# Optimization experiments

Measured on AMD Instinct MI355X. Metric: run time of the kernel, lower is better.

Reference implementation:

```python
import jax, jax.numpy as jnp
import numpy as np

B, N, D_MODEL, H, BLK = 2, 2048, 1024, 16, 128
TB = N // BLK  # 16 blocks per side
NEG = -1e30


def setup_inputs() -> dict:
    key = jax.random.key(0)
    kq, kk, kv, kb = jax.random.split(key, 4)
    q = jax.random.normal(kq, (B, N, D_MODEL), jnp.float32)
    k = jax.random.normal(kk, (B, N, D_MODEL), jnp.float32)
    v = jax.random.normal(kv, (B, N, D_MODEL), jnp.float32)
    tau = jnp.float32(1.0)
    mask = jnp.ones((B, 1, N, N), jnp.int32)
    block_sparse_mask = jax.random.randint(kb, (TB, TB), 0, 2).astype(jnp.int32)
    return {"q": q, "k": k, "v": v, "tau": tau, "mask": mask,
            "block_sparse_mask": block_sparse_mask}


def reference(q, k, v, tau, mask, block_sparse_mask):
    # Equivalent closed form of the tiled online-softmax loop (dropout p=0, eval
    # mode): processed blocks accumulate exactly masked softmax(tau*QK^T/sqrt(dk))@V;
    # rows whose every block is skipped keep O=0, l=0, m=-inf.
    Bq, Nq, D = q.shape
    d_k = D // H
    qh = q.reshape(Bq, Nq, H, d_k).transpose(0, 2, 1, 3)  # (B,H,N,dk)
    kh = k.reshape(Bq, Nq, H, d_k).transpose(0, 2, 1, 3)
    vh = v.reshape(Bq, Nq, H, d_k).transpose(0, 2, 1, 3)

    S = tau * jnp.einsum('bhqd,bhkd->bhqk', qh, kh) / np.sqrt(d_k).astype(np.float32)

    # expand block-sparse pattern to token resolution (N,N)
    bs = jnp.repeat(jnp.repeat(block_sparse_mask, BLK, axis=0), BLK, axis=1)
    allowed = (mask != 0) & (bs != 0)  # (B,1,N,N), broadcasts over heads

    S_m = jnp.where(allowed, S, NEG)
    m = jnp.max(S_m, axis=-1, keepdims=True)            # (B,H,N,1)
    P = jnp.exp(S_m - m) * allowed.astype(S.dtype)      # masked exp-weights
    l = jnp.sum(P, axis=-1, keepdims=True)              # (B,H,N,1)
    Ov = jnp.einsum('bhqk,bhkd->bhqd', P, vh)
    O = Ov / jnp.where(l > 0, l, 1.0)

    has_any = jnp.any(allowed, axis=-1, keepdims=True)  # (B,1,N,1)
    m_out = jnp.where(has_any, m, -jnp.inf)
    O_out = O.transpose(0, 2, 1, 3).reshape(Bq, Nq, D)
    return O_out, l, m_out
```

## Files before the change

### kernel.cpp

```cpp
#include <hip/hip_runtime.h>
#include <hip/hip_bf16.h>

#define B_   2
#define N_   2048
#define DM_  1024
#define H_   16
#define DK_  64
#define BLK_ 128
#define TB_  16

typedef unsigned short u16;
typedef unsigned int   u32;
using bf16x8 = __attribute__((ext_vector_type(8))) __bf16;
using f32x4  = __attribute__((ext_vector_type(4))) float;

#define PPAD 136
#define OPAD 68

__device__ __forceinline__ u32 pack_bf16(float a, float b) {
  __hip_bfloat162 h = __float22bfloat162_rn(make_float2(a, b));
  u32 u; __builtin_memcpy(&u, &h, 4); return u;
}
__device__ __forceinline__ bf16x8 pack8(float4 f0, float4 f1, float sc) {
  u32 w[4];
  w[0] = pack_bf16(f0.x * sc, f0.y * sc); w[1] = pack_bf16(f0.z * sc, f0.w * sc);
  w[2] = pack_bf16(f1.x * sc, f1.y * sc); w[3] = pack_bf16(f1.z * sc, f1.w * sc);
  bf16x8 r; __builtin_memcpy(&r, w, 16); return r;
}

__global__ void prepass_kernel(const float* __restrict__ k, const float* __restrict__ v,
                               const int* __restrict__ mask, const int* __restrict__ bs,
                               u16* __restrict__ kimg, u16* __restrict__ vimg,
                               int* __restrict__ flags) {
  __shared__ u16 tile[BLK_][DK_ + 2];
  __shared__ int sAll[4], sAny[4];
  const int blk0 = blockIdx.x;
  const int t = threadIdx.x;
  if (blk0 < 512) {
    const int nb = blk0 & 15, h = (blk0 >> 4) & 15, b = blk0 >> 8;
    const size_t obase = ((size_t)((b * H_ + h) * TB_ + nb)) * 8192;
    const int rr = t >> 4, cc = (t & 15) * 4;
    {
      const float* kg = k + ((size_t)(b * N_ + nb * BLK_)) * DM_ + h * DK_;
      u16* kd = kimg + obase;
#pragma unroll
      for (int i = 0; i < 8; ++i) {
        const int r = rr + i * 16;
        const float4 f = *(const float4*)(kg + (size_t)r * DM_ + cc);
        const int so = ((((cc >> 3) ^ (r & 7)) << 3) | (cc & 4));
        *(uint2*)(kd + r * 64 + so) = make_uint2(pack_bf16(f.x, f.y), pack_bf16(f.z, f.w));
      }
    }
    {
      const float* vg = v + ((size_t)(b * N_ + nb * BLK_)) * DM_ + h * DK_;
#pragma unroll
      for (int i = 0; i < 8; ++i) {
        const int r = rr + i * 16;
        const float4 f = *(const float4*)(vg + (size_t)r * DM_ + cc);
        *(u32*)(&tile[r][cc])     = pack_bf16(f.x, f.y);
        *(u32*)(&tile[r][cc + 2]) = pack_bf16(f.z, f.w);
      }
      __syncthreads();
      const int d = t & 63, n0 = (t >> 6) * 32;
      u16* og = vimg + obase + d * 128;
#pragma unroll
      for (int j = 0; j < 32; j += 8) {
        u16 tmp[8];
#pragma unroll
        for (int x = 0; x < 8; ++x) tmp[x] = tile[n0 + j + x][d];
        uint4 w; __builtin_memcpy(&w, tmp, 16);
        const int chunk = (n0 + j) >> 3;
        *(uint4*)(og + ((chunk ^ (d & 7)) << 3)) = w;
      }
    }
  } else {
    const int blk = blk0 - 512;
    const int kb = blk % TB_, qb = (blk / TB_) % TB_, b = blk / (TB_ * TB_);
    const int* mg = mask + (size_t)b * N_ * N_ + (size_t)(qb * BLK_) * N_ + kb * BLK_;
    int all1 = 1, any1 = 0;
    for (int i = t; i < BLK_ * BLK_ / 4; i += 256) {
      const int r = i >> 5, c = (i & 31) * 4;
      const int4 mv = *(const int4*)(mg + (size_t)r * N_ + c);
      all1 &= (mv.x != 0) & (mv.y != 0) & (mv.z != 0) & (mv.w != 0);
      any1 |= (mv.x != 0) | (mv.y != 0) | (mv.z != 0) | (mv.w != 0);
    }
    const int wv = t >> 6;
    const int wAll = __all(all1), wAny = __any(any1);
    if ((t & 63) == 0) { sAll[wv] = wAll; sAny[wv] = wAny; }
    __syncthreads();
    if (t == 0) {
      const int A = sAll[0] & sAll[1] & sAll[2] & sAll[3];
      const int O = sAny[0] | sAny[1] | sAny[2] | sAny[3];
      int f = 0;
      if (bs[qb * TB_ + kb] != 0 && O) f = A ? 1 : 2;
      flags[blk] = f;
    }
  }
}

#define SOFTMAX_PHASE(stA, NT) do {                                              \
    if (mix) {                                                                   \
      const int* mg = mask + (size_t)b * N_ * N_ + (size_t)qg[NT] * N_ + cur * BLK_; \
      _Pragma("unroll")                                                          \
      for (int kt = 0; kt < 8; ++kt) {                                           \
        const int4 mv = *(const int4*)(mg + kt * 16 + quad * 4);                 \
        if (!mv.x) stA[kt][0] = -1e30f;                                          \
        if (!mv.y) stA[kt][1] = -1e30f;                                          \
        if (!mv.z) stA[kt][2] = -1e30f;                                          \
        if (!mv.w) stA[kt][3] = -1e30f;                                          \
      }                                                                          \
    }                                                                            \
    float mx = -INFINITY;                                                        \
    _Pragma("unroll")                                                            \
    for (int kt = 0; kt < 8; ++kt)                                               \
      mx = fmaxf(mx, fmaxf(fmaxf(stA[kt][0], stA[kt][1]),                        \
                           fmaxf(stA[kt][2], stA[kt][3])));                      \
    mx = fmaxf(mx, __shfl_xor(mx, 16, 64));                                      \
    mx = fmaxf(mx, __shfl_xor(mx, 32, 64));                                      \
    m_true[NT] = fmaxf(m_true[NT], mx);                                          \
    const float mold = m_run[NT];                                                \
    float mnew = mold;                                                           \
    if (!__all(mx <= mold + 8.f)) {                                              \
      mnew = fmaxf(mold, mx);                                                    \
      const float alpha = __builtin_amdgcn_exp2f(mold - mnew);                   \
      l_run[NT] *= alpha;                                                        \
      _Pragma("unroll")                                                          \
      for (int mt = 0; mt < 4; ++mt)                                             \
        _Pragma("unroll")                                                        \
        for (int r = 0; r < 4; ++r) oacc[NT][mt][r] *= alpha;                    \
      m_run[NT] = mnew;                                                          \
    }                                                                            \
    const int qloc = wave * 32 + NT * 16 + col;                                  \
    float s = 0.f;                                                               \
    if (!mix) {                                                                  \
      _Pragma("unroll")                                                          \
      for (int kt = 0; kt < 8; ++kt) {                                           \
        const float p0 = __builtin_amdgcn_exp2f(stA[kt][0] - mnew);              \
        const float p1 = __builtin_amdgcn_exp2f(stA[kt][1] - mnew);              \
        const float p2 = __builtin_amdgcn_exp2f(stA[kt][2] - mnew);              \
        const float p3 = __builtin_amdgcn_exp2f(stA[kt][3] - mnew);              \
        s += (p0 + p1) + (p2 + p3);                                              \
        *(uint2*)(Ps + qloc * PPAD + kt * 16 + quad * 4) =                       \
            make_uint2(pack_bf16(p0, p1), pack_bf16(p2, p3));                    \
      }                                                                          \
    } else {                                                                     \
      _Pragma("unroll")                                                          \
      for (int kt = 0; kt < 8; ++kt) {                                           \
        const float p0 = stA[kt][0] <= -1e29f ? 0.f : __builtin_amdgcn_exp2f(stA[kt][0] - mnew); \
        const float p1 = stA[kt][1] <= -1e29f ? 0.f : __builtin_amdgcn_exp2f(stA[kt][1] - mnew); \
        const float p2 = stA[kt][2] <= -1e29f ? 0.f : __builtin_amdgcn_exp2f(stA[kt][2] - mnew); \
        const float p3 = stA[kt][3] <= -1e29f ? 0.f : __builtin_amdgcn_exp2f(stA[kt][3] - mnew); \
        s += (p0 + p1) + (p2 + p3);                                              \
        *(uint2*)(Ps + qloc * PPAD + kt * 16 + quad * 4) =                       \
            make_uint2(pack_bf16(p0, p1), pack_bf16(p2, p3));                    \
      }                                                                          \
    }                                                                            \
    s += __shfl_xor(s, 16, 64);                                                  \
    s += __shfl_xor(s, 32, 64);                                                  \
    l_run[NT] += s;                                                              \
  } while (0)

__global__ __launch_bounds__(256, 2)
void attn_kernel(const float* __restrict__ q_, const u16* __restrict__ kimg,
                 const u16* __restrict__ vimg, const float* __restrict__ tau_p,
                 const int* __restrict__ mask, const int* __restrict__ flags,
                 float* __restrict__ o_out, float* __restrict__ l_out,
                 float* __restrict__ m_out) {
  __shared__ __align__(16) u16 lds[8192 + 8192 + BLK_ * PPAD];
  u16* Ps  = lds + 16384;
  float* Os = (float*)lds;

  const int idx = blockIdx.x;
  const int bh = idx & 31, qb128 = idx >> 5;
  const int b = bh >> 4, h = bh & 15;
  const int t = threadIdx.x;
  const int wave = t >> 6, lane = t & 63, quad = lane >> 4, col = lane & 15;

  const int* flg = flags + (b * TB_ + qb128) * TB_;
  u32 actmask = 0, mixmask = 0;
#pragma unroll
  for (int i = 0; i < TB_; ++i) {
    const int f = flg[i];
    actmask |= (f != 0) ? (1u << i) : 0u;
    mixmask |= (f == 2) ? (1u << i) : 0u;
  }

  const u16* kpl = kimg + (size_t)(b * H_ + h) * TB_ * 8192;
  const u16* vpl = vimg + (size_t)(b * H_ + h) * TB_ * 8192;

  int qg[2];
  qg[0] = qb128 * BLK_ + wave * 32 + col;
  qg[1] = qg[0] + 16;

  const float qscale = tau_p[0] * 0.125f * 1.44269504f;
  bf16x8 bq[2][2];
#pragma unroll
  for (int nt = 0; nt < 2; ++nt) {
    const float* qr = q_ + ((size_t)(b * N_ + qg[nt])) * DM_ + h * DK_;
#pragma unroll
    for (int half = 0; half < 2; ++half) {
      const float4 f0 = *(const float4*)(qr + half * 32 + quad * 8);
      const float4 f1 = *(const float4*)(qr + half * 32 + quad * 8 + 4);
      bq[nt][half] = pack8(f0, f1, qscale);
    }
  }

  float m_run[2]  = {-INFINITY, -INFINITY};
  float m_true[2] = {-INFINITY, -INFINITY};
  float l_run[2] = {0.f, 0.f};
  f32x4 oacc[2][4];
#pragma unroll
  for (int nt = 0; nt < 2; ++nt)
#pragma unroll
    for (int mt = 0; mt < 4; ++mt) oacc[nt][mt] = (f32x4){0.f, 0.f, 0.f, 0.f};

  const int s8 = col & 7;
  const int a0o = (quad ^ s8) << 3;

  u32 rem = actmask;
  while (rem) {
    const int cur = (int)__builtin_ctz(rem);
    rem &= rem - 1;
    const int mix = (mixmask >> cur) & 1;

    __syncthreads();
    {
      const u16* ks = kpl + (size_t)cur * 8192;
      const u16* vs = vpl + (size_t)cur * 8192;
      uint4 kr[4], vr[4];
#pragma unroll
      for (int j = 0; j < 4; ++j) {
        const int i = (t + 256 * j) * 8;
        kr[j] = *(const uint4*)(ks + i);
        vr[j] = *(const uint4*)(vs + i);
      }
#pragma unroll
      for (int j = 0; j < 4; ++j) {
        const int i = (t + 256 * j) * 8;
        *(uint4*)(lds + i) = kr[j];
        *(uint4*)(lds + 8192 + i) = vr[j];
      }
    }
    __syncthreads();

    f32x4 st0[8], st1[8];
    __builtin_amdgcn_s_setprio(1);
#pragma unroll
    for (int kt = 0; kt < 8; ++kt) {
      const u16* krow = lds + (kt * 16 + col) * 64;
      const bf16x8 a0 = *(const bf16x8*)(krow + a0o);
      const bf16x8 a1 = *(const bf16x8*)(krow + (a0o ^ 32));
      f32x4 c0 = (f32x4){0.f, 0.f, 0.f, 0.f};
      f32x4 c1 = (f32x4){0.f, 0.f, 0.f, 0.f};
      c0 = __builtin_amdgcn_mfma_f32_16x16x32_bf16(a0, bq[0][0], c0, 0, 0, 0);
      c1 = __builtin_amdgcn_mfma_f32_16x16x32_bf16(a0, bq[1][0], c1, 0, 0, 0);
      c0 = __builtin_amdgcn_mfma_f32_16x16x32_bf16(a1, bq[0][1], c0, 0, 0, 0);
      c1 = __builtin_amdgcn_mfma_f32_16x16x32_bf16(a1, bq[1][1], c1, 0, 0, 0);
      st0[kt] = c0;
      st1[kt] = c1;
    }
    __builtin_amdgcn_s_setprio(0);

    SOFTMAX_PHASE(st0, 0);
    SOFTMAX_PHASE(st1, 1);

    __builtin_amdgcn_s_setprio(1);
#pragma unroll
    for (int ks = 0; ks < 4; ++ks) {
      bf16x8 bfrag[2];
#pragma unroll
      for (int nt = 0; nt < 2; ++nt)
        bfrag[nt] = *(const bf16x8*)(Ps + (wave * 32 + nt * 16 + col) * PPAD + ks * 32 + quad * 8);
#pragma unroll
      for (int mt = 0; mt < 4; ++mt) {
        const bf16x8 av =
            *(const bf16x8*)(lds + 8192 + (mt * 16 + col) * 128 + (((ks * 4 + quad) ^ s8) << 3));
        oacc[0][mt] = __builtin_amdgcn_mfma_f32_16x16x32_bf16(av, bfrag[0], oacc[0][mt], 0, 0, 0);
        oacc[1][mt] = __builtin_amdgcn_mfma_f32_16x16x32_bf16(av, bfrag[1], oacc[1][mt], 0, 0, 0);
      }
    }
    __builtin_amdgcn_s_setprio(0);
  }

  __syncthreads();
#pragma unroll
  for (int nt = 0; nt < 2; ++nt) {
    const float inv = l_run[nt] > 0.f ? 1.f / l_run[nt] : 1.f;
    const int qloc = wave * 32 + nt * 16 + col;
#pragma unroll
    for (int mt = 0; mt < 4; ++mt) {
      float4 w = make_float4(oacc[nt][mt][0] * inv, oacc[nt][mt][1] * inv,
                             oacc[nt][mt][2] * inv, oacc[nt][mt][3] * inv);
      *(float4*)(Os + qloc * OPAD + mt * 16 + quad * 4) = w;
    }
  }
  __syncthreads();
  float* ob = o_out + ((size_t)(b * N_ + qb128 * BLK_)) * DM_ + h * DK_;
#pragma unroll
  for (int j = 0; j < 8; ++j) {
    const int i = t + 256 * j;
    const int r = i >> 4, c4 = (i & 15) * 4;
    const float4 w = *(const float4*)(Os + r * OPAD + c4);
    *(float4*)(ob + (size_t)r * DM_ + c4) = w;
  }
  if (quad == 0) {
#pragma unroll
    for (int nt = 0; nt < 2; ++nt) {
      const size_t oi = (size_t)(b * H_ + h) * N_ + qg[nt];
      const float lv = l_run[nt] > 0.f
          ? l_run[nt] * __builtin_amdgcn_exp2f(m_run[nt] - m_true[nt]) : 0.f;
      l_out[oi] = lv;
      m_out[oi] = l_run[nt] > 0.f ? m_true[nt] * 0.69314718056f : -INFINITY;
    }
  }
}

extern "C" void kernel_launch(void* const* d_in, const int* in_sizes, int n_in,
                              void* d_out, int out_size, void* d_ws, size_t ws_size,
                              hipStream_t stream) {
  const float* q   = (const float*)d_in[0];
  const float* k   = (const float*)d_in[1];
  const float* v   = (const float*)d_in[2];
  const float* tau = (const float*)d_in[3];
  const int* mask  = (const int*)d_in[4];
  const int* bs    = (const int*)d_in[5];
  float* out = (float*)d_out;

  const size_t plane = (size_t)B_ * H_ * N_ * DK_;
  u16* kimg = (u16*)d_ws;
  u16* vimg = kimg + plane;
  int* flags = (int*)(vimg + plane);

  prepass_kernel<<<dim3(1024), 256, 0, stream>>>(k, v, mask, bs, kimg, vimg, flags);

  float* o_out = out;
  float* l_out = out + (size_t)B_ * N_ * DM_;
  float* m_out = l_out + (size_t)B_ * H_ * N_;
  attn_kernel<<<dim3(TB_ * 32), 256, 0, stream>>>(q, kimg, vimg, tau, mask, flags,
                                                  o_out, l_out, m_out);
}
```

Before: 159.7 us.

## Prefetch next K/V block into registers while computing current block

Restructures the block-sparse attention loop so global loads of the next active K/V block are issued into registers before the QK^T, softmax and PV work on the current block. They are written to LDS only after a barrier at the end of the iteration. This hides global-memory latency behind MFMA and softmax work instead of stalling on loads at the start of each iteration. It costs extra live registers (8 uint4 per thread) during compute, which may reduce occupancy, and it does one redundant reload of the last block.

```diff
diff --git a/kernel.cpp b/kernel.cpp
--- a/kernel.cpp
+++ b/kernel.cpp
@@ -97,6 +97,26 @@
     }
   }
 }
+
+#define ISSUE_KV(blk_) do {                                                     \
+    const u16* ks_ = kpl + (size_t)(blk_) * 8192;                               \
+    const u16* vs_ = vpl + (size_t)(blk_) * 8192;                               \
+    _Pragma("unroll")                                                           \
+    for (int j_ = 0; j_ < 4; ++j_) {                                            \
+      const int i_ = (t + 256 * j_) * 8;                                        \
+      kr[j_] = *(const uint4*)(ks_ + i_);                                       \
+      vr[j_] = *(const uint4*)(vs_ + i_);                                       \
+    }                                                                           \
+  } while (0)
+
+#define STAGE_WRITE() do {                                                      \
+    _Pragma("unroll")                                                           \
+    for (int j_ = 0; j_ < 4; ++j_) {                                            \
+      const int i_ = (t + 256 * j_) * 8;                                        \
+      *(uint4*)(lds + i_) = kr[j_];                                             \
+      *(uint4*)(lds + 8192 + i_) = vr[j_];                                      \
+    }                                                                           \
+  } while (0)
 
 #define SOFTMAX_PHASE(stA, NT) do {                                              \
     if (mix) {                                                                   \
@@ -217,69 +237,72 @@
   const int s8 = col & 7;
   const int a0o = (quad ^ s8) << 3;
 
-  u32 rem = actmask;
-  while (rem) {
-    const int cur = (int)__builtin_ctz(rem);
+  if (actmask) {
+    u32 rem = actmask;
+    int cur = (int)__builtin_ctz(rem);
     rem &= rem - 1;
-    const int mix = (mixmask >> cur) & 1;
-
-    __syncthreads();
+
     {
-      const u16* ks = kpl + (size_t)cur * 8192;
-      const u16* vs = vpl + (size_t)cur * 8192;
       uint4 kr[4], vr[4];
-#pragma unroll
-      for (int j = 0; j < 4; ++j) {
-        const int i = (t + 256 * j) * 8;
-        kr[j] = *(const uint4*)(ks + i);
-        vr[j] = *(const uint4*)(vs + i);
-      }
-#pragma unroll
-      for (int j = 0; j < 4; ++j) {
-        const int i = (t + 256 * j) * 8;
-        *(uint4*)(lds + i) = kr[j];
-        *(uint4*)(lds + 8192 + i) = vr[j];
-      }
-    }
-    __syncthreads();
-
-    f32x4 st0[8], st1[8];
-    __builtin_amdgcn_s_setprio(1);
-#pragma unroll
-    for (int kt = 0; kt < 8; ++kt) {
-      const u16* krow = lds + (kt * 16 + col) * 64;
-      const bf16x8 a0 = *(const bf16x8*)(krow + a0o);
-      const bf16x8 a1 = *(const bf16x8*)(krow + (a0o ^ 32));
-      f32x4 c0 = (f32x4){0.f, 0.f, 0.f, 0.f};
-      f32x4 c1 = (f32x4){0.f, 0.f, 0.f, 0.f};
-      c0 = __builtin_amdgcn_mfma_f32_16x16x32_bf16(a0, bq[0][0], c0, 0, 0, 0);
-      c1 = __builtin_amdgcn_mfma_f32_16x16x32_bf16(a0, bq[1][0], c1, 0, 0, 0);
-      c0 = __builtin_amdgcn_mfma_f32_16x16x32_bf16(a1, bq[0][1], c0, 0, 0, 0);
-      c1 = __builtin_amdgcn_mfma_f32_16x16x32_bf16(a1, bq[1][1], c1, 0, 0, 0);
-      st0[kt] = c0;
-      st1[kt] = c1;
-    }
-    __builtin_amdgcn_s_setprio(0);
-
-    SOFTMAX_PHASE(st0, 0);
-    SOFTMAX_PHASE(st1, 1);
-
-    __builtin_amdgcn_s_setprio(1);
-#pragma unroll
-    for (int ks = 0; ks < 4; ++ks) {
-      bf16x8 bfrag[2];
-#pragma unroll
-      for (int nt = 0; nt < 2; ++nt)
-        bfrag[nt] = *(const bf16x8*)(Ps + (wave * 32 + nt * 16 + col) * PPAD + ks * 32 + quad * 8);
-#pragma unroll
-      for (int mt = 0; mt < 4; ++mt) {
-        const bf16x8 av =
-            *(const bf16x8*)(lds + 8192 + (mt * 16 + col) * 128 + (((ks * 4 + quad) ^ s8) << 3));
-        oacc[0][mt] = __builtin_amdgcn_mfma_f32_16x16x32_bf16(av, bfrag[0], oacc[0][mt], 0, 0, 0);
-        oacc[1][mt] = __builtin_amdgcn_mfma_f32_16x16x32_bf16(av, bfrag[1], oacc[1][mt], 0, 0, 0);
-      }
-    }
-    __builtin_amdgcn_s_setprio(0);
+      ISSUE_KV(cur);
+      STAGE_WRITE();
+      __syncthreads();
+    }
+
+    for (;;) {
+      const int more = (rem != 0);
+      const int nxt = more ? (int)__builtin_ctz(rem) : cur;
+      rem = more ? (rem & (rem - 1)) : 0u;
+      const int mix = (mixmask >> cur) & 1;
+
+      uint4 kr[4], vr[4];
+      ISSUE_KV(nxt);
+
+      f32x4 st0[8], st1[8];
+      __builtin_amdgcn_s_setprio(1);
+#pragma unroll
+      for (int kt = 0; kt < 8; ++kt) {
+        const u16* krow = lds + (kt * 16 + col) * 64;
+        const bf16x8 a0 = *(const bf16x8*)(krow + a0o);
+        const bf16x8 a1 = *(const bf16x8*)(krow + (a0o ^ 32));
+        f32x4 c0 = (f32x4){0.f, 0.f, 0.f, 0.f};
+        f32x4 c1 = (f32x4){0.f, 0.f, 0.f, 0.f};
+        c0 = __builtin_amdgcn_mfma_f32_16x16x32_bf16(a0, bq[0][0], c0, 0, 0, 0);
+        c1 = __builtin_amdgcn_mfma_f32_16x16x32_bf16(a0, bq[1][0], c1, 0, 0, 0);
+        c0 = __builtin_amdgcn_mfma_f32_16x16x32_bf16(a1, bq[0][1], c0, 0, 0, 0);
+        c1 = __builtin_amdgcn_mfma_f32_16x16x32_bf16(a1, bq[1][1], c1, 0, 0, 0);
+        st0[kt] = c0;
+        st1[kt] = c1;
+      }
+      __builtin_amdgcn_s_setprio(0);
+
+      SOFTMAX_PHASE(st0, 0);
+      SOFTMAX_PHASE(st1, 1);
+
+      __builtin_amdgcn_s_setprio(1);
+#pragma unroll
+      for (int ks = 0; ks < 4; ++ks) {
+        bf16x8 bfrag[2];
+#pragma unroll
+        for (int nt = 0; nt < 2; ++nt)
+          bfrag[nt] = *(const bf16x8*)(Ps + (wave * 32 + nt * 16 + col) * PPAD + ks * 32 + quad * 8);
+#pragma unroll
+        for (int mt = 0; mt < 4; ++mt) {
+          const bf16x8 av =
+              *(const bf16x8*)(lds + 8192 + (mt * 16 + col) * 128 + (((ks * 4 + quad) ^ s8) << 3));
+          oacc[0][mt] = __builtin_amdgcn_mfma_f32_16x16x32_bf16(av, bfrag[0], oacc[0][mt], 0, 0, 0);
+          oacc[1][mt] = __builtin_amdgcn_mfma_f32_16x16x32_bf16(av, bfrag[1], oacc[1][mt], 0, 0, 0);
+        }
+      }
+      __builtin_amdgcn_s_setprio(0);
+
+      __syncthreads();
+      STAGE_WRITE();
+      __syncthreads();
+
+      cur = nxt;
+      if (!more) break;
+    }
   }
 
   __syncthreads();
```

Result: slower. 187.3 us (+17.2%).
